# Performance work log

Measured on AMD Instinct MI355X. Metric: run time of the kernel, lower is better.

## Reference

```python
import jax, jax.numpy as jnp
import numpy as np

BANDWIDTH_SQ = 1.0   # h^2 = bandwidth**2, bandwidth=1.0
EPS = 0.0            # clamp floor before log (module default)


def setup_inputs() -> dict:
    key = jax.random.key(0)
    k1, k2, k3 = jax.random.split(key, 3)
    X = jax.random.normal(k1, (2048, 16), dtype=jnp.float32)
    data = jax.random.normal(k2, (100000, 16), dtype=jnp.float32)
    sample_weight = jax.random.uniform(k3, (100000,), dtype=jnp.float32)
    return {"X": X, "data": data, "sample_weight": sample_weight}


def reference(X, data, sample_weight):
    # Brute-force ('standard' RootTree returns all points) weighted Gaussian KDE.
    d = X.shape[1]
    # squared distances [Q, N] via expansion (avoids [Q, N, d] intermediate)
    sq = (
        jnp.sum(X * X, axis=-1)[:, None]
        + jnp.sum(data * data, axis=-1)[None, :]
        - 2.0 * (X @ data.T)
    )
    kernel_values = jnp.exp(-0.5 * sq / BANDWIDTH_SQ)  # [Q, N]
    norm_constant = (2.0 * jnp.pi * BANDWIDTH_SQ) ** (-d / 2.0)
    density = (kernel_values @ sample_weight) * norm_constant / jnp.sum(sample_weight)
    log_density = jnp.log(jnp.maximum(density, EPS))
    return log_density
```

## Files before the change

### kernel.cpp

```cpp
#include <hip/hip_runtime.h>

#define D 16
#define WQT 4
#define NCHUNK 256
#define TILES_MAX 25
#define FIN_QPB 64

#define LOG2E 1.4426950408889634f
#define LN2   0.6931471805599453f

typedef __attribute__((ext_vector_type(8))) short bf16x8;
typedef __attribute__((ext_vector_type(4))) float f32x4;

__device__ __forceinline__ unsigned short f2bf(float f) {
    unsigned u = __float_as_uint(f);
    unsigned r = (u + 0x7fffu + ((u >> 16) & 1u)) >> 16;
    return (unsigned short)r;
}

__global__ __launch_bounds__(256, 8) void dens_kernel(
        const float* __restrict__ X, const float* __restrict__ data,
        const float* __restrict__ w, float* __restrict__ part,
        float* __restrict__ wpart, int Q, int N) {
    __shared__ unsigned short sh_hi[(TILES_MAX + 1) * 256];
    __shared__ float          sh_cn[(TILES_MAX + 1) * 16];
    __shared__ float          ls[4];

    const int lane = threadIdx.x & 63;
    const int wave = threadIdx.x >> 6;
    const int col  = lane & 15;
    const int quad = lane >> 4;
    const int koff = (quad & 1) * 8;

    const int qg = blockIdx.x * 4 + wave;

    const int NT = N >> 4;
    const int base = NT / NCHUNK, rem = NT % NCHUNK;
    const int chunk = blockIdx.y;
    const int tile0 = chunk * base + min(chunk, rem);
    const int cnt = base + (chunk < rem ? 1 : 0);
    const int npts = cnt * 16;
    const int n0 = tile0 * 16;

    float ws = 0.f;
    for (int p = threadIdx.x; p < npts; p += 256) {
        const float4* dp = (const float4*)(data + (size_t)(n0 + p) * D);
        float4 v0 = dp[0], v1 = dp[1], v2 = dp[2], v3 = dp[3];
        float vv[16] = {v0.x, v0.y, v0.z, v0.w, v1.x, v1.y, v1.z, v1.w,
                        v2.x, v2.y, v2.z, v2.w, v3.x, v3.y, v3.z, v3.w};
        float dd = 0.f;
        unsigned hp[8];
        #pragma unroll
        for (int j = 0; j < 8; j++) {
            float a = vv[2 * j], b = vv[2 * j + 1];
            dd = fmaf(a, a, fmaf(b, b, dd));
            hp[j] = (unsigned)f2bf(a) | ((unsigned)f2bf(b) << 16);
        }
        uint4* dst = (uint4*)(sh_hi + p * 16);
        dst[0] = make_uint4(hp[0], hp[1], hp[2], hp[3]);
        dst[1] = make_uint4(hp[4], hp[5], hp[6], hp[7]);
        float wn = w[n0 + p];
        ws += wn;
        sh_cn[p] = fmaf(-0.5f * LOG2E, dd, __builtin_amdgcn_logf(wn));
    }
    #pragma unroll
    for (int off = 32; off > 0; off >>= 1) ws += __shfl_down(ws, off, 64);
    if (lane == 0) ls[wave] = ws;

    bf16x8 afrag[WQT];
    #pragma unroll
    for (int t = 0; t < WQT; t++) {
        int q = (qg * WQT + t) * 16 + col;
        const float* xp = X + (size_t)q * D + koff;
        bf16x8 a;
        #pragma unroll
        for (int j = 0; j < 8; j++)
            a[j] = (quad < 2) ? (short)f2bf(xp[j] * LOG2E) : (short)0;
        afrag[t] = a;
    }

    f32x4 dens[WQT];
    #pragma unroll
    for (int t = 0; t < WQT; t++) dens[t] = (f32x4){0.f, 0.f, 0.f, 0.f};

    __syncthreads();

    if (threadIdx.x == 0)
        wpart[chunk] = (ls[0] + ls[1]) + (ls[2] + ls[3]);

    const int eoff = (col << 4) + koff;
    bf16x8 b1 = *(const bf16x8*)(sh_hi + eoff);
    float  c0 = sh_cn[col];
    for (int it = 0; it < cnt; it++) {
        bf16x8 nb1 = *(const bf16x8*)(sh_hi + (it + 1) * 256 + eoff);
        float  nc0 = sh_cn[(it + 1) * 16 + col];
        f32x4 cvec = {c0, c0, c0, c0};
        #pragma unroll
        for (int t = 0; t < WQT; t++) {
            f32x4 s = __builtin_amdgcn_mfma_f32_16x16x32_bf16(afrag[t], b1, cvec, 0, 0, 0);
            f32x4 e;
            #pragma unroll
            for (int r = 0; r < 4; r++)
                e[r] = __builtin_amdgcn_exp2f(s[r]);
            dens[t] += e;
        }
        b1 = nb1; c0 = nc0;
    }

    #pragma unroll
    for (int t = 0; t < WQT; t++) {
        #pragma unroll
        for (int r = 0; r < 4; r++) {
            float v = dens[t][r];
            v += __shfl_xor(v, 1, 64);
            v += __shfl_xor(v, 2, 64);
            v += __shfl_xor(v, 4, 64);
            v += __shfl_xor(v, 8, 64);
            if (col == 0) {
                int q = (qg * WQT + t) * 16 + quad * 4 + r;
                part[(size_t)chunk * Q + q] = v;
            }
        }
    }
}

__global__ __launch_bounds__(256) void fin_kernel(
        const float* __restrict__ X, const float* __restrict__ part,
        const float* __restrict__ wpart, float* __restrict__ out, int Q) {
    __shared__ float sred[4][FIN_QPB];
    __shared__ float swsum;

    const int tid = threadIdx.x;
    const int qi = tid & (FIN_QPB - 1);
    const int seg = tid >> 6;
    const int q = blockIdx.x * FIN_QPB + qi;

    float a0 = 0.f, a1 = 0.f, a2 = 0.f, a3 = 0.f;
    const int c0 = seg * 64;
    #pragma unroll 4
    for (int c = 0; c < 64; c += 4) {
        a0 += part[(size_t)(c0 + c + 0) * Q + q];
        a1 += part[(size_t)(c0 + c + 1) * Q + q];
        a2 += part[(size_t)(c0 + c + 2) * Q + q];
        a3 += part[(size_t)(c0 + c + 3) * Q + q];
    }
    sred[seg][qi] = (a0 + a1) + (a2 + a3);

    if (tid < 64) {
        float wv = (wpart[tid] + wpart[tid + 64]) + (wpart[tid + 128] + wpart[tid + 192]);
        #pragma unroll
        for (int off = 32; off > 0; off >>= 1) wv += __shfl_down(wv, off, 64);
        if (tid == 0) swsum = wv;
    }
    __syncthreads();

    if (tid < FIN_QPB) {
        float dsum = (sred[0][tid] + sred[1][tid]) + (sred[2][tid] + sred[3][tid]);
        int qq = blockIdx.x * FIN_QPB + tid;
        const float4* xp = (const float4*)(X + (size_t)qq * D);
        float4 x0 = xp[0], x1 = xp[1], x2 = xp[2], x3 = xp[3];
        float xx = x0.x*x0.x + x0.y*x0.y + x0.z*x0.z + x0.w*x0.w
                 + x1.x*x1.x + x1.y*x1.y + x1.z*x1.z + x1.w*x1.w
                 + x2.x*x2.x + x2.y*x2.y + x2.z*x2.z + x2.w*x2.w
                 + x3.x*x3.x + x3.y*x3.y + x3.z*x3.z + x3.w*x3.w;
        float aq = -0.5f * LOG2E * xx;
        const float ln_norm = -8.f * 1.8378770664093453f;
        out[qq] = LN2 * (aq + __builtin_amdgcn_logf(dsum)
                            - __builtin_amdgcn_logf(swsum)) + ln_norm;
    }
}

extern "C" void kernel_launch(void* const* d_in, const int* in_sizes, int n_in,
                              void* d_out, int out_size, void* d_ws, size_t ws_size,
                              hipStream_t stream) {
    const float* X    = (const float*)d_in[0];
    const float* data = (const float*)d_in[1];
    const float* w    = (const float*)d_in[2];
    float* out = (float*)d_out;
    int Q = in_sizes[0] / D;
    int N = in_sizes[1] / D;

    float* wpart = (float*)d_ws;
    float* part  = wpart + NCHUNK;

    dim3 grid(Q / (4 * WQT * 16), NCHUNK);
    dens_kernel<<<grid, 256, 0, stream>>>(X, data, w, part, wpart, Q, N);

    fin_kernel<<<Q / FIN_QPB, 256, 0, stream>>>(X, part, wpart, out, Q);
}
```

Before: 108.1 us.

## Fuse final reduction into density kernel via last-block atomic counter

Removes the separate finalize kernel. Each density block increments a per-query-group atomic counter, and the last block to finish for a group reduces all chunk partials and computes the log-density output. This saves a kernel launch and its dependency gap, but adds a memset launch, atomics and fences, and a serial tail in which one block per group reads all 256 partials.

```diff
diff --git a/kernel.cpp b/kernel.cpp
--- a/kernel.cpp
+++ b/kernel.cpp
@@ -4,7 +4,6 @@
 #define WQT 4
 #define NCHUNK 256
 #define TILES_MAX 25
-#define FIN_QPB 64
 
 #define LOG2E 1.4426950408889634f
 #define LN2   0.6931471805599453f
@@ -21,29 +20,34 @@
 __global__ __launch_bounds__(256, 8) void dens_kernel(
         const float* __restrict__ X, const float* __restrict__ data,
         const float* __restrict__ w, float* __restrict__ part,
-        float* __restrict__ wpart, int Q, int N) {
+        float* __restrict__ wpart, unsigned* __restrict__ cnt,
+        float* __restrict__ out, int Q, int N) {
     __shared__ unsigned short sh_hi[(TILES_MAX + 1) * 256];
     __shared__ float          sh_cn[(TILES_MAX + 1) * 16];
     __shared__ float          ls[4];
+    __shared__ float          swsum;
+    __shared__ int            amLast;
 
-    const int lane = threadIdx.x & 63;
-    const int wave = threadIdx.x >> 6;
+    const int tid  = threadIdx.x;
+    const int lane = tid & 63;
+    const int wave = tid >> 6;
     const int col  = lane & 15;
     const int quad = lane >> 4;
     const int koff = (quad & 1) * 8;
 
-    const int qg = blockIdx.x * 4 + wave;
+    const int g  = blockIdx.x;
+    const int qg = g * 4 + wave;
 
     const int NT = N >> 4;
     const int base = NT / NCHUNK, rem = NT % NCHUNK;
     const int chunk = blockIdx.y;
     const int tile0 = chunk * base + min(chunk, rem);
-    const int cnt = base + (chunk < rem ? 1 : 0);
-    const int npts = cnt * 16;
+    const int cntt = base + (chunk < rem ? 1 : 0);
+    const int npts = cntt * 16;
     const int n0 = tile0 * 16;
 
-    float ws = 0.f;
-    for (int p = threadIdx.x; p < npts; p += 256) {
+    float wsl = 0.f;
+    for (int p = tid; p < npts; p += 256) {
         const float4* dp = (const float4*)(data + (size_t)(n0 + p) * D);
         float4 v0 = dp[0], v1 = dp[1], v2 = dp[2], v3 = dp[3];
         float vv[16] = {v0.x, v0.y, v0.z, v0.w, v1.x, v1.y, v1.z, v1.w,
@@ -60,12 +64,12 @@
         dst[0] = make_uint4(hp[0], hp[1], hp[2], hp[3]);
         dst[1] = make_uint4(hp[4], hp[5], hp[6], hp[7]);
         float wn = w[n0 + p];
-        ws += wn;
+        wsl += wn;
         sh_cn[p] = fmaf(-0.5f * LOG2E, dd, __builtin_amdgcn_logf(wn));
     }
     #pragma unroll
-    for (int off = 32; off > 0; off >>= 1) ws += __shfl_down(ws, off, 64);
-    if (lane == 0) ls[wave] = ws;
+    for (int off = 32; off > 0; off >>= 1) wsl += __shfl_down(wsl, off, 64);
+    if (lane == 0) ls[wave] = wsl;
 
     bf16x8 afrag[WQT];
     #pragma unroll
@@ -85,13 +89,13 @@
 
     __syncthreads();
 
-    if (threadIdx.x == 0)
+    if (tid == 0)
         wpart[chunk] = (ls[0] + ls[1]) + (ls[2] + ls[3]);
 
     const int eoff = (col << 4) + koff;
     bf16x8 b1 = *(const bf16x8*)(sh_hi + eoff);
     float  c0 = sh_cn[col];
-    for (int it = 0; it < cnt; it++) {
+    for (int it = 0; it < cntt; it++) {
         bf16x8 nb1 = *(const bf16x8*)(sh_hi + (it + 1) * 256 + eoff);
         float  nc0 = sh_cn[(it + 1) * 16 + col];
         f32x4 cvec = {c0, c0, c0, c0};
@@ -122,29 +126,17 @@
             }
         }
     }
-}
 
-__global__ __launch_bounds__(256) void fin_kernel(
-        const float* __restrict__ X, const float* __restrict__ part,
-        const float* __restrict__ wpart, float* __restrict__ out, int Q) {
-    __shared__ float sred[4][FIN_QPB];
-    __shared__ float swsum;
-
-    const int tid = threadIdx.x;
-    const int qi = tid & (FIN_QPB - 1);
-    const int seg = tid >> 6;
-    const int q = blockIdx.x * FIN_QPB + qi;
-
-    float a0 = 0.f, a1 = 0.f, a2 = 0.f, a3 = 0.f;
-    const int c0 = seg * 64;
-    #pragma unroll 4
-    for (int c = 0; c < 64; c += 4) {
-        a0 += part[(size_t)(c0 + c + 0) * Q + q];
-        a1 += part[(size_t)(c0 + c + 1) * Q + q];
-        a2 += part[(size_t)(c0 + c + 2) * Q + q];
-        a3 += part[(size_t)(c0 + c + 3) * Q + q];
+    __syncthreads();
+    if (tid == 0) {
+        __threadfence();
+        unsigned prev = __hip_atomic_fetch_add(&cnt[g], 1u, __ATOMIC_ACQ_REL,
+                                               __HIP_MEMORY_SCOPE_AGENT);
+        amLast = (prev == NCHUNK - 1);
     }
-    sred[seg][qi] = (a0 + a1) + (a2 + a3);
+    __syncthreads();
+    if (!amLast) return;
+    __threadfence();
 
     if (tid < 64) {
         float wv = (wpart[tid] + wpart[tid + 64]) + (wpart[tid + 128] + wpart[tid + 192]);
@@ -154,20 +146,28 @@
     }
     __syncthreads();
 
-    if (tid < FIN_QPB) {
-        float dsum = (sred[0][tid] + sred[1][tid]) + (sred[2][tid] + sred[3][tid]);
-        int qq = blockIdx.x * FIN_QPB + tid;
-        const float4* xp = (const float4*)(X + (size_t)qq * D);
-        float4 x0 = xp[0], x1 = xp[1], x2 = xp[2], x3 = xp[3];
-        float xx = x0.x*x0.x + x0.y*x0.y + x0.z*x0.z + x0.w*x0.w
-                 + x1.x*x1.x + x1.y*x1.y + x1.z*x1.z + x1.w*x1.w
-                 + x2.x*x2.x + x2.y*x2.y + x2.z*x2.z + x2.w*x2.w
-                 + x3.x*x3.x + x3.y*x3.y + x3.z*x3.z + x3.w*x3.w;
-        float aq = -0.5f * LOG2E * xx;
-        const float ln_norm = -8.f * 1.8378770664093453f;
-        out[qq] = LN2 * (aq + __builtin_amdgcn_logf(dsum)
-                            - __builtin_amdgcn_logf(swsum)) + ln_norm;
+    const int qq = g * 256 + tid;
+    float a8[8];
+    #pragma unroll
+    for (int u = 0; u < 8; u++) a8[u] = 0.f;
+    for (int c = 0; c < NCHUNK; c += 8) {
+        #pragma unroll
+        for (int u = 0; u < 8; u++)
+            a8[u] += part[(size_t)(c + u) * Q + qq];
     }
+    float dsum = ((a8[0] + a8[1]) + (a8[2] + a8[3]))
+               + ((a8[4] + a8[5]) + (a8[6] + a8[7]));
+
+    const float4* xp = (const float4*)(X + (size_t)qq * D);
+    float4 x0 = xp[0], x1 = xp[1], x2 = xp[2], x3 = xp[3];
+    float xx = x0.x*x0.x + x0.y*x0.y + x0.z*x0.z + x0.w*x0.w
+             + x1.x*x1.x + x1.y*x1.y + x1.z*x1.z + x1.w*x1.w
+             + x2.x*x2.x + x2.y*x2.y + x2.z*x2.z + x2.w*x2.w
+             + x3.x*x3.x + x3.y*x3.y + x3.z*x3.z + x3.w*x3.w;
+    float aq = -0.5f * LOG2E * xx;
+    const float ln_norm = -8.f * 1.8378770664093453f;
+    out[qq] = LN2 * (aq + __builtin_amdgcn_logf(dsum)
+                        - __builtin_amdgcn_logf(swsum)) + ln_norm;
 }
 
 extern "C" void kernel_launch(void* const* d_in, const int* in_sizes, int n_in,
@@ -180,11 +180,12 @@
     int Q = in_sizes[0] / D;
     int N = in_sizes[1] / D;
 
-    float* wpart = (float*)d_ws;
-    float* part  = wpart + NCHUNK;
+    unsigned* cnt  = (unsigned*)d_ws;
+    float* wpart   = (float*)d_ws + 8;
+    float* part    = wpart + NCHUNK;
+
+    hipMemsetAsync(cnt, 0, 8 * sizeof(unsigned), stream);
 
     dim3 grid(Q / (4 * WQT * 16), NCHUNK);
-    dens_kernel<<<grid, 256, 0, stream>>>(X, data, w, part, wpart, Q, N);
-
-    fin_kernel<<<Q / FIN_QPB, 256, 0, stream>>>(X, part, wpart, out, Q);
+    dens_kernel<<<grid, 256, 0, stream>>>(X, data, w, part, wpart, cnt, out, Q, N);
 }
```

After: 213.2 us. +97.2%, slower.
